# Performance work log

Hardware: AMD Instinct MI355X
Metric: run time of the kernel (lower is better)

## Reference

```python
import jax, jax.numpy as jnp
import numpy as np

D_MODEL = 1024
D_FFN = 4096
H = 16
D_HEAD = D_MODEL // H
B, L = 2, 2048
EPS = 1e-6


def layer_norm(x, a, b):
    # Matches torch: std is unbiased (ddof=1), and divides by (std + eps)
    mean = jnp.mean(x, axis=-1, keepdims=True)
    var = jnp.sum((x - mean) ** 2, axis=-1, keepdims=True) / (x.shape[-1] - 1)
    std = jnp.sqrt(var)
    return (x - mean) / (std + EPS) * a + b


def setup_inputs() -> dict:
    key = jax.random.key(0)
    ks = jax.random.split(key, 10)
    s = 0.02
    x = jax.random.normal(ks[0], (B, L, D_MODEL), dtype=jnp.float32)
    mask = jnp.tril(jnp.ones((L, L), dtype=jnp.int32))[None, None]  # causal [1,1,L,L]
    return {
        "x": x,
        "mask": mask,
        "Wqkv": jax.random.normal(ks[1], (D_MODEL, 3 * D_MODEL), jnp.float32) * s,
        "bqkv": jnp.zeros((3 * D_MODEL,), jnp.float32),
        "Wo": jax.random.normal(ks[2], (D_MODEL, D_MODEL), jnp.float32) * s,
        "bo": jnp.zeros((D_MODEL,), jnp.float32),
        "W1": jax.random.normal(ks[3], (D_MODEL, D_FFN), jnp.float32) * s,
        "b1": jnp.zeros((D_FFN,), jnp.float32),
        "W2": jax.random.normal(ks[4], (D_FFN, D_MODEL), jnp.float32) * s,
        "b2": jnp.zeros((D_MODEL,), jnp.float32),
        "ln1_a": jnp.ones((D_MODEL,), jnp.float32),
        "ln1_b": jnp.zeros((D_MODEL,), jnp.float32),
        "ln2_a": jnp.ones((D_MODEL,), jnp.float32),
        "ln2_b": jnp.zeros((D_MODEL,), jnp.float32),
    }


def reference(x, mask, Wqkv, bqkv, Wo, bo, W1, b1, W2, b2, ln1_a, ln1_b, ln2_a, ln2_b):
    b, l, d = x.shape
    # --- attention sublayer ---
    qkv = x @ Wqkv + bqkv                                   # [b, l, 3*d]
    qkv = qkv.reshape(b, l, 3, H, D_HEAD)                   # '(three h d)' ordering
    q, k, v = qkv[:, :, 0], qkv[:, :, 1], qkv[:, :, 2]      # each [b, l, h, dh]
    scores = jnp.einsum('bqhd,bkhd->bhqk', q, k) / jnp.sqrt(
        jnp.asarray(D_HEAD, x.dtype))                        # [b, h, lq, lk]
    scores = jnp.where(mask == 0, -jnp.inf, scores)
    p = jax.nn.softmax(scores, axis=-1)
    attn = jnp.einsum('bhqk,bkhd->bqhd', p, v).reshape(b, l, d)
    attn_out = attn @ Wo + bo
    x = layer_norm(x + attn_out, ln1_a, ln1_b)
    # --- MLP sublayer ---
    h = jax.nn.relu(x @ W1 + b1)
    mlp_out = h @ W2 + b2
    return layer_norm(x + mlp_out, ln2_a, ln2_b)
```

## Files before the change

kernel.cpp:

```cpp
#include <hip/hip_runtime.h>

#define D_MODEL 1024
#define D_FFN   4096
#define NH      16
#define DH      64
#define BB      2
#define LL      2048
#define MROWS   (BB * LL)

typedef unsigned short u16;
typedef unsigned int   u32;
typedef short bf16x8 __attribute__((ext_vector_type(8)));
typedef float f32x4  __attribute__((ext_vector_type(4)));

__device__ __forceinline__ float bf2f(u16 u) {
    union { u32 i; float f; } v;
    v.i = ((u32)u) << 16;
    return v.f;
}
__device__ __forceinline__ u16 f2bf(float f) {
    union { float f; u32 i; } v;
    v.f = f;
    u32 x = v.i;
    x += 0x7fffu + ((x >> 16) & 1u);
    return (u16)(x >> 16);
}
__device__ __forceinline__ u32 pack_bf_trunc(float a, float b) {
    return __builtin_amdgcn_perm(__float_as_uint(b), __float_as_uint(a),
                                 0x07060302u);
}

typedef const __attribute__((address_space(1))) u32 gu32;
typedef __attribute__((address_space(3))) u32 lu32;
__device__ __forceinline__ void gload_lds16(const void* g, void* l) {
    __builtin_amdgcn_global_load_lds((gu32*)g, (lu32*)l, 16, 0, 0);
}

__device__ __forceinline__ void wt_tile(
    const float* __restrict__ W, u16* __restrict__ Wt,
    int K, int N, int t, int tid, float* tile )
{
    const int ntiles = N >> 6;
    const int n0 = (t % ntiles) * 64;
    const int k0 = (t / ntiles) * 64;

    int kr = tid >> 4;
    int nc = (tid & 15) * 4;
    #pragma unroll
    for (int p = 0; p < 4; ++p) {
        float4 v = *(const float4*)&W[(size_t)(k0 + kr + p * 16) * N + n0 + nc];
        tile[(kr + p * 16) * 65 + nc + 0] = v.x;
        tile[(kr + p * 16) * 65 + nc + 1] = v.y;
        tile[(kr + p * 16) * 65 + nc + 2] = v.z;
        tile[(kr + p * 16) * 65 + nc + 3] = v.w;
    }
    __syncthreads();

    int nr = tid >> 2;
    int kc = (tid & 3) * 16;
    u16 o[16];
    #pragma unroll
    for (int j = 0; j < 16; ++j) o[j] = f2bf(tile[(kc + j) * 65 + nr]);
    u16* dst = &Wt[(size_t)(n0 + nr) * K + k0 + kc];
    *(uint4*)dst       = *(const uint4*)&o[0];
    *(uint4*)(dst + 8) = *(const uint4*)&o[8];
}

__global__ __launch_bounds__(256) void prep_kernel(
    const float* __restrict__ x,    u16* __restrict__ xb,
    const float* __restrict__ Wqkv, u16* __restrict__ Wqkvt)
{
    __shared__ float tile[64 * 65];
    const int tid = threadIdx.x;
    const int bi  = blockIdx.x;

    if (bi < 2048) {
        int i = bi * 2048 + tid * 8;
        float4 a = *(const float4*)(x + i);
        float4 b = *(const float4*)(x + i + 4);
        u16 o[8] = {f2bf(a.x), f2bf(a.y), f2bf(a.z), f2bf(a.w),
                    f2bf(b.x), f2bf(b.y), f2bf(b.z), f2bf(b.w)};
        *(uint4*)(xb + i) = *(const uint4*)o;
        return;
    }
    wt_tile(Wqkv, Wqkvt, 1024, 3072, bi - 2048, tid, tile);
}

template <int EPI, int RF32, int OF32, int KS>
__global__ __launch_bounds__(256, 4) void gemm_bt_kernel(
    const u16* __restrict__ A, const u16* __restrict__ Bt,
    const float* __restrict__ bias, const void* __restrict__ resv,
    void* __restrict__ out0v, u16* __restrict__ out1, u16* __restrict__ out2,
    int M, int N, int K)
{
    __shared__ u16 smem[16384];
    u16* sA = smem;
    u16* sB = smem + 8192;

    const int tid  = threadIdx.x;
    const int lane = tid & 63;
    const int wave = tid >> 6;
    const int wm   = (wave & 1) * 64;
    const int wn   = (wave >> 1) * 64;
    const int quad = lane >> 4;
    const int l16  = lane & 15;

    const int nb  = gridDim.x;
    const int mb  = gridDim.y;
    const int f   = blockIdx.y * nb + blockIdx.x;
    const int xcd = f & 7;
    const int idx = f >> 3;
    const int rn  = nb >> 1;
    const int rm  = mb >> 2;
    const int n0  = ((xcd & 1) * rn + (idx % rn)) * 128;
    const int ym  = (xcd >> 1) * rm + (idx / rn);

    int s, m0;
    if (KS > 1) {
        const int mt = mb / KS;
        s  = ym / mt;
        m0 = (ym % mt) * 128;
    } else {
        s  = 0;
        m0 = ym * 128;
    }
    const int Kseg = K / KS;
    const int kbeg = s * Kseg;

    f32x4 acc[4][4];
    #pragma unroll
    for (int i = 0; i < 4; ++i)
        #pragma unroll
        for (int j = 0; j < 4; ++j)
            acc[i][j] = (f32x4){0.f, 0.f, 0.f, 0.f};

    const u16* Ablk = A  + (size_t)m0 * K;
    const u16* Bblk = Bt + (size_t)n0 * K;

    for (int k0 = kbeg; k0 < kbeg + Kseg; k0 += 64) {
        #pragma unroll
        for (int i = 0; i < 4; ++i) {
            int chunk = (i * 4 + wave) * 64 + lane;
            int r = chunk >> 3;
            int c = (chunk & 7) ^ (r & 7);
            size_t goff = (size_t)r * K + k0 + c * 8;
            gload_lds16(Ablk + goff, &sA[(i * 4 + wave) * 512]);
            gload_lds16(Bblk + goff, &sB[(i * 4 + wave) * 512]);
        }
        __syncthreads();

        #pragma unroll
        for (int ks = 0; ks < 2; ++ks) {
            bf16x8 af[4], bfr[4];
            #pragma unroll
            for (int i = 0; i < 4; ++i) {
                int R = wm + i * 16 + l16;
                int slot = R * 8 + ((ks * 4 + quad) ^ (R & 7));
                af[i] = *(const bf16x8*)&sA[slot * 8];
            }
            #pragma unroll
            for (int j = 0; j < 4; ++j) {
                int R = wn + j * 16 + l16;
                int slot = R * 8 + ((ks * 4 + quad) ^ (R & 7));
                bfr[j] = *(const bf16x8*)&sB[slot * 8];
            }
            #pragma unroll
            for (int i = 0; i < 4; ++i)
                #pragma unroll
                for (int j = 0; j < 4; ++j)
                    acc[i][j] = __builtin_amdgcn_mfma_f32_16x16x32_bf16(
                        af[i], bfr[j], acc[i][j], 0, 0, 0);
        }
        __syncthreads();
    }

    if (EPI == 0 && n0 >= 2 * D_MODEL) {
        u16* tile = smem;
        #pragma unroll
        for (int i = 0; i < 4; ++i) {
            int rl = wm + i * 16 + quad * 4;
            #pragma unroll
            for (int j = 0; j < 4; ++j) {
                int cl = wn + j * 16 + l16;
                float bv = bias[n0 + cl];
                int sx = 8 * (cl & 15);
                #pragma unroll
                for (int r = 0; r < 4; ++r)
                    tile[cl * 128 + ((rl + r) ^ sx)] = f2bf(acc[i][j][r] + bv);
            }
        }
        __syncthreads();
        int cl  = tid >> 1;
        int rb  = (tid & 1) * 64;
        int col = n0 + cl;
        int h   = (col >> 6) & 15;
        int d   = col & 63;
        int b   = m0 >> 11;
        int l0  = (m0 & 2047) + rb;
        int sx  = 8 * (cl & 15);
        u16* dst = out2 + ((size_t)(b * NH + h) * DH + d) * LL + l0;
        #pragma unroll
        for (int u = 0; u < 8; ++u) {
            uint4 q = *(const uint4*)&tile[cl * 128 + ((rb + 8 * u) ^ sx)];
            *(uint4*)(dst + 8 * u) = q;
        }
        return;
    }

    #pragma unroll
    for (int i = 0; i < 4; ++i) {
        int rowb = m0 + wm + i * 16 + quad * 4;
        #pragma unroll
        for (int j = 0; j < 4; ++j) {
            int col = n0 + wn + j * 16 + l16;
            float bv = (EPI == 3) ? 0.f : bias[col];
            #pragma unroll
            for (int r = 0; r < 4; ++r) {
                int rr = rowb + r;
                float v = acc[i][j][r] + bv;
                if (EPI == 0) {
                    int h     = (col >> 6) & 15;
                    int d     = col & 63;
                    int b     = rr >> 11;
                    int l     = rr & 2047;
                    size_t idx2 = ((size_t)(b * NH + h) * LL + l) * DH + d;
                    u16* o0 = (u16*)out0v;
                    if (col < D_MODEL)  o0[idx2]   = f2bf(v * 0.18033688f);
                    else                out1[idx2] = f2bf(v);
                } else if (EPI == 3) {
                    ((u16*)out0v)[((size_t)s * M + rr) * N + col] = f2bf(v);
                } else {
                    size_t idx2 = (size_t)rr * N + col;
                    if (EPI == 1) {
                        v += RF32 ? ((const float*)resv)[idx2]
                                  : bf2f(((const u16*)resv)[idx2]);
                    } else {
                        v = v > 0.f ? v : 0.f;
                    }
                    if (OF32) ((float*)out0v)[idx2] = v;
                    else      ((u16*)out0v)[idx2]   = f2bf(v);
                }
            }
        }
    }
}

template <int KS, int RF32, int OF32>
__global__ __launch_bounds__(256) void lnfuse_kernel(
    const u16* __restrict__ P, const float* __restrict__ bias,
    const void* __restrict__ resv,
    const float* __restrict__ ga, const float* __restrict__ gb,
    void* __restrict__ outv)
{
    __shared__ float red[8];
    const int tid  = threadIdx.x;
    const int lane = tid & 63;
    const int wave = tid >> 6;
    const size_t row = blockIdx.x;
    const size_t SL  = (size_t)MROWS * D_MODEL;
    const int c = tid * 4;

    float v0, v1, v2, v3;
    {
        float4 bv = *(const float4*)(bias + c);
        v0 = bv.x; v1 = bv.y; v2 = bv.z; v3 = bv.w;
    }
    #pragma unroll
    for (int s = 0; s < KS; ++s) {
        uint2 p = *(const uint2*)(P + s * SL + row * D_MODEL + c);
        v0 += bf2f((u16)p.x); v1 += bf2f((u16)(p.x >> 16));
        v2 += bf2f((u16)p.y); v3 += bf2f((u16)(p.y >> 16));
    }
    if (RF32) {
        float4 r = *(const float4*)((const float*)resv + row * D_MODEL + c);
        v0 += r.x; v1 += r.y; v2 += r.z; v3 += r.w;
    } else {
        uint2 r = *(const uint2*)((const u16*)resv + row * D_MODEL + c);
        v0 += bf2f((u16)r.x); v1 += bf2f((u16)(r.x >> 16));
        v2 += bf2f((u16)r.y); v3 += bf2f((u16)(r.y >> 16));
    }

    float s_ = v0 + v1 + v2 + v3;
    #pragma unroll
    for (int o = 32; o > 0; o >>= 1) s_ += __shfl_xor(s_, o, 64);
    if (lane == 0) red[wave] = s_;
    __syncthreads();
    float mean = (red[0] + red[1] + red[2] + red[3]) * (1.f / 1024.f);

    float d0 = v0 - mean, d1 = v1 - mean, d2 = v2 - mean, d3 = v3 - mean;
    float q = d0 * d0 + d1 * d1 + d2 * d2 + d3 * d3;
    #pragma unroll
    for (int o = 32; o > 0; o >>= 1) q += __shfl_xor(q, o, 64);
    if (lane == 0) red[4 + wave] = q;
    __syncthreads();
    float var = (red[4] + red[5] + red[6] + red[7]) * (1.f / 1023.f);
    float inv = 1.f / (sqrtf(var) + 1e-6f);

    float y0 = d0 * inv * ga[c + 0] + gb[c + 0];
    float y1 = d1 * inv * ga[c + 1] + gb[c + 1];
    float y2 = d2 * inv * ga[c + 2] + gb[c + 2];
    float y3 = d3 * inv * ga[c + 3] + gb[c + 3];
    if (OF32) {
        float4 y = {y0, y1, y2, y3};
        *(float4*)((float*)outv + row * D_MODEL + c) = y;
    } else {
        ushort4 y = {f2bf(y0), f2bf(y1), f2bf(y2), f2bf(y3)};
        *(ushort4*)((u16*)outv + row * D_MODEL + c) = y;
    }
}

__global__ __launch_bounds__(256) void attn_kernel(
    const u16* __restrict__ Q, const u16* __restrict__ K,
    const u16* __restrict__ V, u16* __restrict__ out,
    const float* __restrict__ Wo, u16* __restrict__ Wot,
    const float* __restrict__ W1, u16* __restrict__ W1t,
    const float* __restrict__ W2, u16* __restrict__ W2t)
{
    __shared__ u16 smem[13824];
    u16* ks = smem;
    u16* vs = smem + 4608;
    u16* ps = smem + 9216;

    const int tid  = threadIdx.x;
    const int bi   = blockIdx.x;

    if (bi >= 1024) {
        float* tile = (float*)smem;
        int t = bi - 1024;
        if (t < 256)       wt_tile(Wo, Wot, 1024, 1024, t,        tid, tile);
        else if (t < 1280) wt_tile(W1, W1t, 1024, 4096, t - 256,  tid, tile);
        else               wt_tile(W2, W2t, 4096, 1024, t - 1280, tid, tile);
        return;
    }

    const int lane = tid & 63;
    const int wave = tid >> 6;
    const int l16  = lane & 15;
    const int quad = lane >> 4;

    const int xcd = bi & 7;
    const int idx = bi >> 3;
    const int bh  = xcd * 4 + (idx & 3);
    const int j   = idx >> 2;
    const int qt  = (j < 16) ? (31 - j) : (j - 16);
    const int b   = bh >> 4, h = bh & 15;
    const size_t head_off = (size_t)bh * LL * DH;

    const u16* Qh = Q + head_off;
    const u16* Kh = K + head_off;
    const u16* Vh = V + head_off;

    const int base = qt * 64 + wave * 16;
    const int qg   = base + l16;

    const bf16x8 qf0 = *(const bf16x8*)&Qh[(size_t)qg * DH + quad * 8];
    const bf16x8 qf1 = *(const bf16x8*)&Qh[(size_t)qg * DH + 32 + quad * 8];

    float lsum = 0.f;
    f32x4 o[4];
    #pragma unroll
    for (int t = 0; t < 4; ++t) o[t] = (f32x4){0.f, 0.f, 0.f, 0.f};

    u16* psw = ps + wave * 1152;

    const int key = tid >> 2;
    const int kd0 = (tid & 3) * 16;

    const int vC    = 4 * ((key >> 3) & 7);
    const int vbase = (kd0 >> 1) ^ (vC & 24);
    const int vofA  = vbase + (vC & 4);
    const int vofB  = vbase + ((vC & 4) ^ 4);
    u32* vs32 = (u32*)vs;

    uint4 kr0, kr1, vr0, vr1;
    {
        const u16* ksrc = Kh + (size_t)key * DH + kd0;
        kr0 = *(const uint4*)ksrc;
        kr1 = *(const uint4*)(ksrc + 8);
        const u16* vsrc = Vh + (size_t)key * LL + kd0;
        vr0 = *(const uint4*)vsrc;
        vr1 = *(const uint4*)(vsrc + 8);
    }

    for (int c = 0; c <= qt; ++c) {
        __syncthreads();
        *(uint4*)&ks[key * 72 + kd0]     = kr0;
        *(uint4*)&ks[key * 72 + kd0 + 8] = kr1;
        *(uint4*)&vs32[key * 36 + vofA]  = vr0;
        *(uint4*)&vs32[key * 36 + vofB]  = vr1;
        __syncthreads();
        if (c < qt) {
            const u16* ksrc = Kh + (size_t)((c + 1) * 64 + key) * DH + kd0;
            kr0 = *(const uint4*)ksrc;
            kr1 = *(const uint4*)(ksrc + 8);
            const u16* vsrc = Vh + (size_t)key * LL + (c + 1) * 64 + kd0;
            vr0 = *(const uint4*)vsrc;
            vr1 = *(const uint4*)(vsrc + 8);
        }

        f32x4 st[4];
        #pragma unroll
        for (int t = 0; t < 4; ++t) {
            bf16x8 k0 = *(const bf16x8*)&ks[(t * 16 + l16) * 72 + quad * 8];
            bf16x8 k1 = *(const bf16x8*)&ks[(t * 16 + l16) * 72 + 32 + quad * 8];
            f32x4 s = (f32x4){0.f, 0.f, 0.f, 0.f};
            s = __builtin_amdgcn_mfma_f32_16x16x32_bf16(k0, qf0, s, 0, 0, 0);
            s = __builtin_amdgcn_mfma_f32_16x16x32_bf16(k1, qf1, s, 0, 0, 0);
            st[t] = s;
        }

        if (c == qt) {
            #pragma unroll
            for (int t = 0; t < 4; ++t)
                #pragma unroll
                for (int r = 0; r < 4; ++r)
                    if (c * 64 + t * 16 + quad * 4 + r > qg) st[t][r] = -INFINITY;
        }

        {
            float psum = 0.f;
            #pragma unroll
            for (int t = 0; t < 4; ++t) {
                float p0 = exp2f(st[t][0]), p1 = exp2f(st[t][1]);
                float p2 = exp2f(st[t][2]), p3 = exp2f(st[t][3]);
                psum += (p0 + p1) + (p2 + p3);
                uint2 w = {pack_bf_trunc(p0, p1), pack_bf_trunc(p2, p3)};
                *(uint2*)&psw[l16 * 72 + t * 16 + quad * 4] = w;
            }
            psum += __shfl_xor(psum, 16, 64);
            psum += __shfl_xor(psum, 32, 64);
            lsum += psum;
        }

        bf16x8 pf0 = *(const bf16x8*)&psw[l16 * 72 + quad * 8];
        bf16x8 pf1 = *(const bf16x8*)&psw[l16 * 72 + 32 + quad * 8];

        #pragma unroll
        for (int dt = 0; dt < 4; ++dt) {
            int d  = dt * 16 + l16;
            int sw = 4 * ((d >> 3) & 7);
            bf16x8 vf0 = *(const bf16x8*)&vs[d * 72 + 2 * ((quad * 4) ^ sw)];
            bf16x8 vf1 = *(const bf16x8*)&vs[d * 72 + 2 * ((16 + quad * 4) ^ sw)];
            o[dt] = __builtin_amdgcn_mfma_f32_16x16x32_bf16(pf0, vf0, o[dt], 0, 0, 0);
            o[dt] = __builtin_amdgcn_mfma_f32_16x16x32_bf16(pf1, vf1, o[dt], 0, 0, 0);
        }
    }

    {
        float i0 = 1.f / __shfl(lsum, quad * 4 + 0, 64);
        float i1 = 1.f / __shfl(lsum, quad * 4 + 1, 64);
        float i2 = 1.f / __shfl(lsum, quad * 4 + 2, 64);
        float i3 = 1.f / __shfl(lsum, quad * 4 + 3, 64);
        #pragma unroll
        for (int dt = 0; dt < 4; ++dt) {
            size_t col = h * DH + dt * 16 + l16;
            size_t r0  = ((size_t)b * LL + base + quad * 4) * D_MODEL + col;
            out[r0]               = f2bf(o[dt][0] * i0);
            out[r0 + D_MODEL]     = f2bf(o[dt][1] * i1);
            out[r0 + 2 * D_MODEL] = f2bf(o[dt][2] * i2);
            out[r0 + 3 * D_MODEL] = f2bf(o[dt][3] * i3);
        }
    }
}

extern "C" void kernel_launch(void* const* d_in, const int* in_sizes, int n_in,
                              void* d_out, int out_size, void* d_ws, size_t ws_size,
                              hipStream_t stream)
{
    const float* x    = (const float*)d_in[0];
    const float* Wqkv = (const float*)d_in[2];
    const float* bqkv = (const float*)d_in[3];
    const float* Wo   = (const float*)d_in[4];
    const float* bo   = (const float*)d_in[5];
    const float* W1   = (const float*)d_in[6];
    const float* b1   = (const float*)d_in[7];
    const float* W2   = (const float*)d_in[8];
    const float* b2   = (const float*)d_in[9];
    const float* ln1a = (const float*)d_in[10];
    const float* ln1b = (const float*)d_in[11];
    const float* ln2a = (const float*)d_in[12];
    const float* ln2b = (const float*)d_in[13];

    char* ws = (char*)d_ws;
    const size_t HSZ = (size_t)BB * NH * LL * DH;
    u16*   Qp    = (u16*)ws;
    u16*   Kp    = Qp + HSZ;
    u16*   Vp    = Kp + HSZ;
    u16*   attn  = Vp + HSZ;
    u16*   hbuf  = (u16*)ws;
    u16*   xb    = (u16*)(ws + 33554432);
    u16*   x1    = (u16*)(ws + 50331648);
    u16*   Wqkvt = (u16*)(ws + 58720256);
    u16*   Wot   = (u16*)(ws + 65011712);
    u16*   W1t   = (u16*)(ws + 67108864);
    u16*   W2t   = (u16*)(ws + 75497472);
    u16*   Pbuf  = (u16*)(ws + 83886080);

    dim3 blk(256);

    prep_kernel<<<dim3(2816), blk, 0, stream>>>(x, xb, Wqkv, Wqkvt);

    gemm_bt_kernel<0,0,0,1><<<dim3(24, 32), blk, 0, stream>>>(
        xb, Wqkvt, bqkv, nullptr, Qp, Kp, Vp, MROWS, 3 * D_MODEL, D_MODEL);
    attn_kernel<<<dim3(3328), blk, 0, stream>>>(
        Qp, Kp, Vp, attn, Wo, Wot, W1, W1t, W2, W2t);
    gemm_bt_kernel<3,0,0,2><<<dim3(8, 64), blk, 0, stream>>>(
        attn, Wot, bo, nullptr, Pbuf, nullptr, nullptr, MROWS, D_MODEL, D_MODEL);
    lnfuse_kernel<2,1,0><<<dim3(MROWS), blk, 0, stream>>>(
        Pbuf, bo, x, ln1a, ln1b, x1);
    gemm_bt_kernel<2,0,0,1><<<dim3(32, 32), blk, 0, stream>>>(
        x1, W1t, b1, nullptr, hbuf, nullptr, nullptr, MROWS, D_FFN, D_MODEL);
    gemm_bt_kernel<3,0,0,4><<<dim3(8, 128), blk, 0, stream>>>(
        hbuf, W2t, b2, nullptr, Pbuf, nullptr, nullptr, MROWS, D_MODEL, D_FFN);
    lnfuse_kernel<4,0,1><<<dim3(MROWS), blk, 0, stream>>>(
        Pbuf, b2, x1, ln2a, ln2b, d_out);
}
```

Measured before the change: 314.5 us.

## Add 256x256-tile 512-thread GEMM kernel for the MLP GEMMs

Introduces a new bf16 MFMA GEMM kernel with 256x256 output tiles, 8 waves, double-buffered direct-to-LDS loads with an XOR swizzle, and an XCD-aware block remap. It replaces the previous 128-tile GEMM for the W1 (ReLU) and split-K W2 projections. Larger tiles raise arithmetic intensity and cut global traffic per FLOP. The cost is higher register and LDS pressure (128 KB LDS per block, 128 accumulator floats per thread), and the W1 launch has only 256 blocks, which may underfill the device.

```diff
diff --git a/kernel.cpp b/kernel.cpp
--- a/kernel.cpp
+++ b/kernel.cpp
@@ -245,6 +245,132 @@
     }
 }
 
+template <int EPI, int KS>
+__global__ __launch_bounds__(512, 2) void gemm256_kernel(
+    const u16* __restrict__ A, const u16* __restrict__ Bt,
+    const float* __restrict__ bias, void* __restrict__ outv,
+    int M, int N, int K)
+{
+    __shared__ u16 dsm[65536];
+
+    const int tid  = threadIdx.x;
+    const int lane = tid & 63;
+    const int wave = tid >> 6;
+    const int wm   = wave >> 2;
+    const int wn   = wave & 3;
+    const int quad = lane >> 4;
+    const int l16  = lane & 15;
+
+    const int nb  = gridDim.x;
+    const int mb  = gridDim.y;
+    const int f   = blockIdx.y * nb + blockIdx.x;
+    const int xcd = f & 7;
+    const int idx = f >> 3;
+    const int rn  = nb >> 1;
+    const int rm  = mb >> 2;
+    const int n0  = ((xcd & 1) * rn + (idx % rn)) * 256;
+    const int ym  = (xcd >> 1) * rm + (idx / rn);
+
+    int s, m0;
+    if (KS > 1) {
+        const int mt = mb / KS;
+        s  = ym / mt;
+        m0 = (ym % mt) * 256;
+    } else {
+        s  = 0;
+        m0 = ym * 256;
+    }
+    const int Kseg = K / KS;
+    const int kbeg = s * Kseg;
+    const int NT   = Kseg >> 6;
+
+    const int rr = tid >> 3;
+    const int cc = ((tid & 7) ^ (rr & 7)) * 8;
+    const u16* Asrc[4];
+    const u16* Bsrc[4];
+    #pragma unroll
+    for (int q = 0; q < 4; ++q) {
+        Asrc[q] = A  + (size_t)(m0 + q * 64 + rr) * K + kbeg + cc;
+        Bsrc[q] = Bt + (size_t)(n0 + q * 64 + rr) * K + kbeg + cc;
+    }
+
+    f32x4 acc[8][4];
+    #pragma unroll
+    for (int i = 0; i < 8; ++i)
+        #pragma unroll
+        for (int j = 0; j < 4; ++j)
+            acc[i][j] = (f32x4){0.f, 0.f, 0.f, 0.f};
+
+    #pragma unroll
+    for (int q = 0; q < 4; ++q) {
+        gload_lds16(Asrc[q], &dsm[q * 4096 + wave * 512]);
+        gload_lds16(Bsrc[q], &dsm[16384 + q * 4096 + wave * 512]);
+    }
+
+    #pragma unroll 1
+    for (int kt = 0; kt < NT; ++kt) {
+        u16* nbuf = &dsm[((kt + 1) & 1) * 32768];
+        if (kt + 1 < NT) {
+            int koff = (kt + 1) * 64;
+            #pragma unroll
+            for (int q = 0; q < 4; ++q) {
+                gload_lds16(Asrc[q] + koff, nbuf + q * 4096 + wave * 512);
+                gload_lds16(Bsrc[q] + koff, nbuf + 16384 + q * 4096 + wave * 512);
+            }
+            asm volatile("s_waitcnt vmcnt(8)" ::: "memory");
+        } else {
+            asm volatile("s_waitcnt vmcnt(0)" ::: "memory");
+        }
+        asm volatile("s_barrier" ::: "memory");
+        __builtin_amdgcn_sched_barrier(0);
+
+        const u16* sAc = &dsm[(kt & 1) * 32768];
+        const u16* sBc = sAc + 16384;
+        #pragma unroll
+        for (int ks = 0; ks < 2; ++ks) {
+            bf16x8 af[8], bfr[4];
+            #pragma unroll
+            for (int i = 0; i < 8; ++i) {
+                int R = wm * 128 + i * 16 + l16;
+                af[i] = *(const bf16x8*)&sAc[(R * 8 + ((ks * 4 + quad) ^ (l16 & 7))) * 8];
+            }
+            #pragma unroll
+            for (int j = 0; j < 4; ++j) {
+                int R = wn * 64 + j * 16 + l16;
+                bfr[j] = *(const bf16x8*)&sBc[(R * 8 + ((ks * 4 + quad) ^ (l16 & 7))) * 8];
+            }
+            #pragma unroll
+            for (int i = 0; i < 8; ++i)
+                #pragma unroll
+                for (int j = 0; j < 4; ++j)
+                    acc[i][j] = __builtin_amdgcn_mfma_f32_16x16x32_bf16(
+                        af[i], bfr[j], acc[i][j], 0, 0, 0);
+        }
+        __builtin_amdgcn_sched_barrier(0);
+        asm volatile("s_barrier" ::: "memory");
+    }
+
+    #pragma unroll
+    for (int i = 0; i < 8; ++i) {
+        int rowb = m0 + wm * 128 + i * 16 + quad * 4;
+        #pragma unroll
+        for (int j = 0; j < 4; ++j) {
+            int col = n0 + wn * 64 + j * 16 + l16;
+            float bv = (EPI == 3) ? 0.f : bias[col];
+            #pragma unroll
+            for (int r = 0; r < 4; ++r) {
+                float v = acc[i][j][r] + bv;
+                if (EPI == 2) {
+                    v = v > 0.f ? v : 0.f;
+                    ((u16*)outv)[(size_t)(rowb + r) * N + col] = f2bf(v);
+                } else {
+                    ((u16*)outv)[((size_t)s * M + rowb + r) * N + col] = f2bf(v);
+                }
+            }
+        }
+    }
+}
+
 template <int KS, int RF32, int OF32>
 __global__ __launch_bounds__(256) void lnfuse_kernel(
     const u16* __restrict__ P, const float* __restrict__ bias,
@@ -508,10 +634,10 @@
         attn, Wot, bo, nullptr, Pbuf, nullptr, nullptr, MROWS, D_MODEL, D_MODEL);
     lnfuse_kernel<2,1,0><<<dim3(MROWS), blk, 0, stream>>>(
         Pbuf, bo, x, ln1a, ln1b, x1);
-    gemm_bt_kernel<2,0,0,1><<<dim3(32, 32), blk, 0, stream>>>(
-        x1, W1t, b1, nullptr, hbuf, nullptr, nullptr, MROWS, D_FFN, D_MODEL);
-    gemm_bt_kernel<3,0,0,4><<<dim3(8, 128), blk, 0, stream>>>(
-        hbuf, W2t, b2, nullptr, Pbuf, nullptr, nullptr, MROWS, D_MODEL, D_FFN);
+    gemm256_kernel<2,1><<<dim3(16, 16), dim3(512), 0, stream>>>(
+        x1, W1t, b1, hbuf, MROWS, D_FFN, D_MODEL);
+    gemm256_kernel<3,4><<<dim3(4, 64), dim3(512), 0, stream>>>(
+        hbuf, W2t, nullptr, Pbuf, MROWS, D_MODEL, D_FFN);
     lnfuse_kernel<4,0,1><<<dim3(MROWS), blk, 0, stream>>>(
         Pbuf, b2, x1, ln2a, ln2b, d_out);
 }
```

New measurement: 314.0 us. No clear change (-0.2%).
